# Kernel optimization log

Measured on AMD Instinct MI355X. Metric: run time of the kernel, lower is better.

Reference implementation:

```python
import jax, jax.numpy as jnp
import numpy as np

B, S, D, H = 2, 2048, 1024, 16
HD = D // H


def setup_inputs() -> dict:
    key = jax.random.key(0)
    ks = jax.random.split(key, 6)
    std = 1.0 / np.sqrt(D)
    return {
        "hidden_states": jax.random.normal(ks[0], (B, S, D), dtype=jnp.float32),
        "attention_mask": jnp.zeros((B, 1, S, S), dtype=jnp.float32),
        "Wq": jax.random.normal(ks[1], (D, D), dtype=jnp.float32) * std,
        "bq": jnp.zeros((D,), dtype=jnp.float32),
        "Wk": jax.random.normal(ks[2], (D, D), dtype=jnp.float32) * std,
        "bk": jnp.zeros((D,), dtype=jnp.float32),
        "Wv": jax.random.normal(ks[3], (D, D), dtype=jnp.float32) * std,
        "bv": jnp.zeros((D,), dtype=jnp.float32),
        "Wo": jax.random.normal(ks[4], (D, D), dtype=jnp.float32) * std,
        "bo": jnp.zeros((D,), dtype=jnp.float32),
    }


def reference(hidden_states, attention_mask, Wq, bq, Wk, bk, Wv, bv, Wo, bo):
    scale = HD ** (-0.5)
    # torch Linear: y = x @ W^T + b
    def proj(x, W, b):
        y = jnp.einsum('bsd,ed->bse', x, W) + b
        return y.reshape(B, S, H, HD).transpose(0, 2, 1, 3)  # [B,H,S,HD]
    q = proj(hidden_states, Wq, bq)
    k = proj(hidden_states, Wk, bk)
    v = proj(hidden_states, Wv, bv)
    scores = jnp.einsum('bhqd,bhkd->bhqk', q, k) * scale + attention_mask
    attn = jax.nn.softmax(scores, axis=-1)  # dropout p=0.0 -> identity
    out = jnp.einsum('bhqk,bhkd->bhqd', attn, v)
    out = out.transpose(0, 2, 1, 3).reshape(B, S, D)
    return jnp.einsum('bsd,ed->bse', out, Wo) + bo
```

## Files before the change

kernel.cpp:

```cpp
#include <hip/hip_runtime.h>
#include <hip/hip_bf16.h>
#include <stdint.h>

#define Bb 2
#define Ss 2048
#define Dd 1024
#define Hh 16
#define HD 64

typedef __attribute__((ext_vector_type(8))) __bf16 bf16x8;
typedef __attribute__((ext_vector_type(4))) __bf16 bf16x4;
typedef __attribute__((ext_vector_type(2))) __bf16 bf16x2;
typedef __attribute__((ext_vector_type(4))) float f32x4;
typedef __attribute__((ext_vector_type(16))) float f32x16;

#define LOG2E 1.44269504088896f
#define SCL2 (0.125f * LOG2E)

#define HS_N   (Bb * Ss * Dd)
#define W_N    (Dd * Dd)
#define B_N    (Dd)
#define MS_N   ((long)Bb * Ss * Ss)
#define CAN_HS 0
#define CAN_WQ (CAN_HS + HS_N)
#define CAN_BQ (CAN_WQ + W_N)
#define CAN_WK (CAN_BQ + B_N)
#define CAN_BK (CAN_WK + W_N)
#define CAN_WV (CAN_BK + B_N)
#define CAN_BV (CAN_WV + W_N)
#define CAN_WO (CAN_BV + B_N)
#define CAN_BO (CAN_WO + W_N)
#define CAN_END (CAN_BO + B_N)
#define TSZ    (Bb * Hh * Ss * HD)
#define WS_ELEMS (CAN_END + 4 * TSZ)
#define WS_NEED ((size_t)WS_ELEMS * 2)

__device__ __forceinline__ void gl_lds16(const __bf16* g, __bf16* l) {
  __builtin_amdgcn_global_load_lds(
      (const __attribute__((address_space(1))) void*)g,
      (__attribute__((address_space(3))) void*)l,
      16, 0, 0);
}

__device__ __forceinline__ void cfence() { asm volatile("" ::: "memory"); }

__global__ void canon_kernel(const float* hs, const float* Wq, const float* bq,
                             const float* Wk, const float* bk, const float* Wv,
                             const float* bv, const float* Wo, const float* bo,
                             __bf16* __restrict__ dst,
                             const float* __restrict__ Mf,
                             __bf16* __restrict__ mout) {
  const float* srcs[9] = {hs, Wq, bq, Wk, bk, Wv, bv, Wo, bo};
  const long starts[10] = {CAN_HS, CAN_WQ, CAN_BQ, CAN_WK, CAN_BK,
                           CAN_WV, CAN_BV, CAN_WO, CAN_BO, CAN_END};
  const long nA = CAN_END / 8;
  const long nTot = nA + MS_N / 8;
  for (long c = blockIdx.x * blockDim.x + threadIdx.x; c < nTot;
       c += (long)gridDim.x * blockDim.x) {
    if (c < nA) {
      const long i = c * 8;
      int seg = 0;
#pragma unroll
      for (int t = 1; t < 9; t++) seg += (i >= starts[t]) ? 1 : 0;
      const float* s = srcs[seg] + (i - starts[seg]);
      bf16x8 v;
#pragma unroll
      for (int e = 0; e < 8; e++) v[e] = (__bf16)s[e];
      *(bf16x8*)(dst + i) = v;
    } else {
      const long i = (c - nA) * 8;
      const float* s = Mf + i;
      bf16x8 v;
#pragma unroll
      for (int e = 0; e < 8; e++) v[e] = (__bf16)(s[e] * LOG2E);
      *(bf16x8*)(mout + i) = v;
    }
  }
}

template <int MODE, typename OutT>
__global__ __launch_bounds__(256, 2) void gemm_bt(
    const __bf16* __restrict__ A,
    const __bf16* __restrict__ W0, const __bf16* __restrict__ W1,
    const __bf16* __restrict__ W2,
    const __bf16* __restrict__ b0, const __bf16* __restrict__ b1,
    const __bf16* __restrict__ b2,
    OutT* __restrict__ O0, OutT* __restrict__ O1, OutT* __restrict__ O2) {
  __shared__ __align__(16) __bf16 sA[2][128 * 32];
  __shared__ __align__(16) __bf16 sB[2][128 * 32];
  const int tid = threadIdx.x;
  const int lane = tid & 63;
  const int wid = tid >> 6;
  const int quad = lane >> 4;
  const int l15 = lane & 15;
  const int mBlock = blockIdx.x * 128;

  const __bf16* W;
  const __bf16* bias;
  OutT* Out;
  int nBlock, which = 0;
  if (MODE == 0) {
    which = blockIdx.y >> 3;
    nBlock = (blockIdx.y & 7) * 128;
    W = which == 0 ? W0 : (which == 1 ? W1 : W2);
    bias = which == 0 ? b0 : (which == 1 ? b1 : b2);
    Out = which == 0 ? O0 : (which == 1 ? O1 : O2);
  } else {
    nBlock = blockIdx.y * 128;
    W = W0;
    bias = b0;
    Out = O0;
  }

  const int waveM = (wid >> 1) * 64;
  const int waveN = (wid & 1) * 64;

  f32x4 acc[4][4] = {};

  const int c1 = wid * 64 + lane;
  const int c2 = c1 + 256;
  const __bf16* Ar1 = A + (mBlock + (c1 >> 2)) * Dd + (c1 & 3) * 8;
  const __bf16* Ar2 = A + (mBlock + (c2 >> 2)) * Dd + (c2 & 3) * 8;
  const __bf16* Wr1 = W + (nBlock + (c1 >> 2)) * Dd + (c1 & 3) * 8;
  const __bf16* Wr2 = W + (nBlock + (c2 >> 2)) * Dd + (c2 & 3) * 8;
  const int d1 = (wid * 64) * 8;
  const int d2 = (wid * 64 + 256) * 8;

#define GSTAGE(BI, K0)                                                        \
  {                                                                           \
    gl_lds16(Ar1 + (K0), sA[BI] + d1);                                        \
    gl_lds16(Ar2 + (K0), sA[BI] + d2);                                        \
    gl_lds16(Wr1 + (K0), sB[BI] + d1);                                        \
    gl_lds16(Wr2 + (K0), sB[BI] + d2);                                        \
  }

  GSTAGE(0, 0);

#pragma unroll 2
  for (int kt = 0; kt < 32; ++kt) {
    const int bufc = kt & 1;
    __syncthreads();
    if (kt < 31) {
      GSTAGE(bufc ^ 1, (kt + 1) * 32);
    }

    bf16x8 aF[4], bF[4];
#pragma unroll
    for (int mi = 0; mi < 4; mi++)
      aF[mi] =
          *(const bf16x8*)(sA[bufc] + (waveM + mi * 16 + l15) * 32 + quad * 8);
#pragma unroll
    for (int ni = 0; ni < 4; ni++)
      bF[ni] =
          *(const bf16x8*)(sB[bufc] + (waveN + ni * 16 + l15) * 32 + quad * 8);
#pragma unroll
    for (int mi = 0; mi < 4; mi++)
#pragma unroll
      for (int ni = 0; ni < 4; ni++)
        acc[mi][ni] = __builtin_amdgcn_mfma_f32_16x16x32_bf16(
            aF[mi], bF[ni], acc[mi][ni], 0, 0, 0);
  }

#pragma unroll
  for (int ni = 0; ni < 4; ni++) {
    const int ng = nBlock + waveN + ni * 16 + l15;
    const float bv = (float)bias[ng];
#pragma unroll
    for (int mi = 0; mi < 4; mi++) {
      const int mg0 = mBlock + waveM + mi * 16 + quad * 4;
      if (MODE == 0 && which == 2) {
        const int b = mg0 >> 11, s0 = mg0 & 2047;
        const int h = ng >> 6, hd = ng & 63;
        bf16x4 pk;
#pragma unroll
        for (int r = 0; r < 4; r++) pk[r] = (__bf16)(acc[mi][ni][r] + bv);
        *(bf16x4*)((__bf16*)Out + (((b * Hh + h) * HD + hd) * Ss) + s0) = pk;
      } else {
#pragma unroll
        for (int r = 0; r < 4; r++) {
          float v = acc[mi][ni][r] + bv;
          const int m = mg0 + r;
          if (MODE == 0) {
            if (which == 0) v *= SCL2;
            const int b = m >> 11, s = m & 2047;
            const int h = ng >> 6, hd = ng & 63;
            Out[(((b * Hh + h) * Ss + s) * HD) + hd] = (OutT)v;
          } else {
            Out[m * Dd + ng] = (OutT)v;
          }
        }
      }
    }
  }
}

__global__ __launch_bounds__(256, 4) void attn_fused(
    const __bf16* __restrict__ Qg, const __bf16* __restrict__ Kg,
    const __bf16* __restrict__ Vt, const __bf16* __restrict__ Mbf,
    __bf16* __restrict__ Og) {
  __shared__ __align__(16) union {
    struct {
      __bf16 kv[2][8192];
      __bf16 mk[4096];
    } s;
    struct {
      float O[2][64][32];
      float L[2][32];
    } m;
  } sh;

  const int tid = threadIdx.x;
  const int lane = tid & 63;
  const int wid = tid >> 6;
  const int qg = wid & 1;
  const int kvh = wid >> 1;
  const int l31 = lane & 31;
  const int hi = lane >> 5;

  const int id = blockIdx.x;
  const int j = id >> 3;
  const int bh = (id & 7) * 4 + (j >> 5);
  const int qb0 = (j & 31) * 64;
  const int b = bh >> 4;
  const int h = bh & 15;
  const int qw = qb0 + qg * 32 + l31;

  const __bf16* Qp = Qg + (size_t)bh * Ss * HD;
  const __bf16* Kp = Kg + (size_t)bh * Ss * HD;
  const __bf16* Vp = Vt + (size_t)bh * HD * Ss;
  const __bf16* Mb = Mbf + (size_t)b * Ss * Ss;

  bf16x8 qf[4];
#pragma unroll
  for (int k = 0; k < 4; k++)
    qf[k] = *(const bf16x8*)(Qp + (size_t)qw * HD + k * 16 + hi * 8);

  const int cA = tid, cB = 256 + tid;
#define STAGE_KV(BI, KVS)                                                     \
  {                                                                           \
    const int rwA = (cA & 255) >> 2, rwB = (cB & 255) >> 2;                   \
    const int slA = (cA & 3) ^ ((rwA >> 1) & 3);                              \
    const int slB = (cB & 3) ^ ((rwB >> 1) & 3);                              \
    __bf16* kb = sh.s.kv[BI];                                                 \
    gl_lds16(Kp + ((KVS) + rwA) * HD + (cA >> 8) * 32 + slA * 8, kb + cA * 8);\
    gl_lds16(Kp + ((KVS) + rwB) * HD + (cB >> 8) * 32 + slB * 8, kb + cB * 8);\
    __bf16* vb = sh.s.kv[BI] + 4096;                                          \
    gl_lds16(Vp + (size_t)rwA * Ss + (KVS) + (cA >> 8) * 32 + slA * 8,        \
             vb + cA * 8);                                                    \
    gl_lds16(Vp + (size_t)rwB * Ss + (KVS) + (cB >> 8) * 32 + slB * 8,        \
             vb + cB * 8);                                                    \
  }

#define STAGE_M(KVS)                                                          \
  {                                                                           \
    _Pragma("unroll")                                                         \
    for (int rr = 0; rr < 2; rr++) {                                          \
      const int c = tid + rr * 256;                                           \
      const int mq = c >> 3;                                                  \
      const int l8 = (c & 7) ^ (mq & 7);                                      \
      gl_lds16(Mb + (size_t)(qb0 + mq) * Ss + (KVS) + l8 * 8,                 \
               sh.s.mk + c * 8);                                              \
    }                                                                         \
  }

  f32x16 o[2] = {};
  f32x4 lacc = {0.f, 0.f, 0.f, 0.f};

  const int rsw = (l31 >> 1) & 3;

  STAGE_KV(0, 0);
  STAGE_M(0);

  for (int it = 0; it < 32; ++it) {
    const int bufc = it & 1;
    cfence();
    asm volatile("s_waitcnt vmcnt(0)" ::: "memory");
    cfence();
    __builtin_amdgcn_s_barrier();
    cfence();
    if (it < 31) {
      STAGE_KV(bufc ^ 1, (it + 1) * 64);
      cfence();
    }

    bf16x4 mcv[4];
    const int mq = qg * 32 + l31;
#pragma unroll
    for (int g = 0; g < 4; g++) {
      const int p8 = (4 * kvh + g) ^ (l31 & 7);
      mcv[g] = *(const bf16x4*)(sh.s.mk + mq * 64 + p8 * 8 + 4 * hi);
    }
    cfence();
    asm volatile("s_waitcnt lgkmcnt(0)" ::: "memory");
    cfence();
    __builtin_amdgcn_s_barrier();
    cfence();
    if (it < 31) {
      STAGE_M((it + 1) * 64);
      cfence();
    }

    f32x16 sacc;
#pragma unroll
    for (int g = 0; g < 4; g++)
#pragma unroll
      for (int r = 0; r < 4; r++) sacc[g * 4 + r] = (float)mcv[g][r];
    __builtin_amdgcn_s_setprio(1);
#pragma unroll
    for (int k = 0; k < 4; k++) {
      const int ps = (((k & 1) << 1) | hi) ^ rsw;
      bf16x8 kf = *(const bf16x8*)(sh.s.kv[bufc] +
                                   ((k >> 1) * 64 + kvh * 32 + l31) * 32 +
                                   ps * 8);
      sacc = __builtin_amdgcn_mfma_f32_32x32x16_bf16(kf, qf[k], sacc, 0, 0, 0);
    }
    __builtin_amdgcn_s_setprio(0);

    f32x4 sv[4];
#pragma unroll
    for (int g = 0; g < 4; g++)
#pragma unroll
      for (int r = 0; r < 4; r++)
        sv[g][r] = __builtin_amdgcn_exp2f(sacc[g * 4 + r]);
    lacc += (sv[0] + sv[1]) + (sv[2] + sv[3]);

    union pu { bf16x4 v; uint32_t w[2]; };
    pu pk[4];
#pragma unroll
    for (int g = 0; g < 4; g++)
#pragma unroll
      for (int r = 0; r < 4; r++) pk[g].v[r] = (__bf16)sv[g][r];
    union PF { bf16x8 v; uint32_t u[4]; } pf[2];
#pragma unroll
    for (int ks = 0; ks < 2; ks++) {
      uint32_t a0 = pk[2 * ks].w[0], b0 = pk[2 * ks + 1].w[0];
      uint32_t a1 = pk[2 * ks].w[1], b1 = pk[2 * ks + 1].w[1];
      asm volatile("s_nop 1\n\tv_permlane32_swap_b32 %0, %1"
                   : "+v"(a0), "+v"(b0));
      asm volatile("s_nop 1\n\tv_permlane32_swap_b32 %0, %1"
                   : "+v"(a1), "+v"(b1));
      pf[ks].u[0] = a0;
      pf[ks].u[1] = a1;
      pf[ks].u[2] = b0;
      pf[ks].u[3] = b1;
    }

    __builtin_amdgcn_s_setprio(1);
#pragma unroll
    for (int k = 0; k < 2; k++)
#pragma unroll
      for (int hb = 0; hb < 2; hb++) {
        const int ps = ((k << 1) | hi) ^ rsw;
        bf16x8 vf = *(const bf16x8*)(sh.s.kv[bufc] + 4096 +
                                     (kvh * 64 + hb * 32 + l31) * 32 +
                                     ps * 8);
        o[hb] = __builtin_amdgcn_mfma_f32_32x32x16_bf16(vf, pf[k].v, o[hb],
                                                        0, 0, 0);
      }
    __builtin_amdgcn_s_setprio(0);
  }

  float l = lacc[0] + lacc[1] + lacc[2] + lacc[3];
  l += __shfl_xor(l, 32);

  __syncthreads();
  if (kvh == 1) {
#pragma unroll
    for (int hb = 0; hb < 2; hb++)
#pragma unroll
      for (int r = 0; r < 16; r++) {
        const int hd = hb * 32 + (r & 3) + 8 * (r >> 2) + 4 * hi;
        sh.m.O[qg][hd][l31] = o[hb][r];
      }
    if (hi == 0) sh.m.L[qg][l31] = l;
  }
  __syncthreads();
  if (kvh == 0) {
#pragma unroll
    for (int hb = 0; hb < 2; hb++)
#pragma unroll
      for (int r = 0; r < 16; r++) {
        const int hd = hb * 32 + (r & 3) + 8 * (r >> 2) + 4 * hi;
        o[hb][r] += sh.m.O[qg][hd][l31];
      }
    l += sh.m.L[qg][l31];
    const float inv = 1.0f / l;
    __bf16* Ow = Og + (((size_t)b * Ss + qw) * Hh + h) * HD;
#pragma unroll
    for (int hb = 0; hb < 2; hb++)
#pragma unroll
      for (int g = 0; g < 4; g++) {
        const int hd = hb * 32 + g * 8 + 4 * hi;
        bf16x2 w0, w1;
        w0[0] = (__bf16)(o[hb][g * 4 + 0] * inv);
        w0[1] = (__bf16)(o[hb][g * 4 + 1] * inv);
        w1[0] = (__bf16)(o[hb][g * 4 + 2] * inv);
        w1[1] = (__bf16)(o[hb][g * 4 + 3] * inv);
        *(bf16x2*)(Ow + hd) = w0;
        *(bf16x2*)(Ow + hd + 2) = w1;
      }
  }
}

extern "C" void kernel_launch(void* const* d_in, const int* in_sizes, int n_in,
                              void* d_out, int out_size, void* d_ws,
                              size_t ws_size, hipStream_t stream) {
  if (ws_size < WS_NEED) return;

  __bf16* ws = (__bf16*)d_ws;
  const __bf16* hsC = ws + CAN_HS;
  const __bf16* WqC = ws + CAN_WQ;
  const __bf16* bqC = ws + CAN_BQ;
  const __bf16* WkC = ws + CAN_WK;
  const __bf16* bkC = ws + CAN_BK;
  const __bf16* WvC = ws + CAN_WV;
  const __bf16* bvC = ws + CAN_BV;
  const __bf16* WoC = ws + CAN_WO;
  const __bf16* boC = ws + CAN_BO;
  __bf16* Q = ws + CAN_END;
  __bf16* K = Q + TSZ;
  __bf16* V = K + TSZ;
  __bf16* AW = V + TSZ;
  float* out = (float*)d_out;
  __bf16* Mbf = (__bf16*)d_out;

  canon_kernel<<<2048, 256, 0, stream>>>(
      (const float*)d_in[0], (const float*)d_in[2], (const float*)d_in[3],
      (const float*)d_in[4], (const float*)d_in[5], (const float*)d_in[6],
      (const float*)d_in[7], (const float*)d_in[8], (const float*)d_in[9], ws,
      (const float*)d_in[1], Mbf);
  gemm_bt<0, __bf16><<<dim3(32, 24), 256, 0, stream>>>(
      hsC, WqC, WkC, WvC, bqC, bkC, bvC, Q, K, V);
  attn_fused<<<dim3(1024), 256, 0, stream>>>(Q, K, V, Mbf, AW);
  gemm_bt<1, float><<<dim3(32, 8), 256, 0, stream>>>(
      AW, WoC, WoC, WoC, boC, boC, boC, out, out, out);
}
```

Before: 226.4 us.

## Overlap mask conversion with QKV GEMM and narrow output-GEMM tiles

The fp32-to-bf16 mask conversion moves out of the canonicalisation kernel into 256 extra blocks of the QKV projection GEMM, so it runs alongside the matmul blocks instead of serially before them. Separately, the output projection GEMM uses 128x64 tiles instead of 128x128, doubling its grid from 256 to 512 blocks to fill more compute units. The trade-off is lower per-block data reuse in the output GEMM, and mask blocks competing with GEMM blocks for bandwidth and scheduling slots.

```diff
diff --git a/kernel.cpp b/kernel.cpp
--- a/kernel.cpp
+++ b/kernel.cpp
@@ -47,34 +47,22 @@
 __global__ void canon_kernel(const float* hs, const float* Wq, const float* bq,
                              const float* Wk, const float* bk, const float* Wv,
                              const float* bv, const float* Wo, const float* bo,
-                             __bf16* __restrict__ dst,
-                             const float* __restrict__ Mf,
-                             __bf16* __restrict__ mout) {
+                             __bf16* __restrict__ dst) {
   const float* srcs[9] = {hs, Wq, bq, Wk, bk, Wv, bv, Wo, bo};
   const long starts[10] = {CAN_HS, CAN_WQ, CAN_BQ, CAN_WK, CAN_BK,
                            CAN_WV, CAN_BV, CAN_WO, CAN_BO, CAN_END};
   const long nA = CAN_END / 8;
-  const long nTot = nA + MS_N / 8;
-  for (long c = blockIdx.x * blockDim.x + threadIdx.x; c < nTot;
+  for (long c = blockIdx.x * blockDim.x + threadIdx.x; c < nA;
        c += (long)gridDim.x * blockDim.x) {
-    if (c < nA) {
-      const long i = c * 8;
-      int seg = 0;
-#pragma unroll
-      for (int t = 1; t < 9; t++) seg += (i >= starts[t]) ? 1 : 0;
-      const float* s = srcs[seg] + (i - starts[seg]);
-      bf16x8 v;
-#pragma unroll
-      for (int e = 0; e < 8; e++) v[e] = (__bf16)s[e];
-      *(bf16x8*)(dst + i) = v;
-    } else {
-      const long i = (c - nA) * 8;
-      const float* s = Mf + i;
-      bf16x8 v;
-#pragma unroll
-      for (int e = 0; e < 8; e++) v[e] = (__bf16)(s[e] * LOG2E);
-      *(bf16x8*)(mout + i) = v;
-    }
+    const long i = c * 8;
+    int seg = 0;
+#pragma unroll
+    for (int t = 1; t < 9; t++) seg += (i >= starts[t]) ? 1 : 0;
+    const float* s = srcs[seg] + (i - starts[seg]);
+    bf16x8 v;
+#pragma unroll
+    for (int e = 0; e < 8; e++) v[e] = (__bf16)s[e];
+    *(bf16x8*)(dst + i) = v;
   }
 }
 
@@ -85,10 +73,27 @@
     const __bf16* __restrict__ W2,
     const __bf16* __restrict__ b0, const __bf16* __restrict__ b1,
     const __bf16* __restrict__ b2,
-    OutT* __restrict__ O0, OutT* __restrict__ O1, OutT* __restrict__ O2) {
+    OutT* __restrict__ O0, OutT* __restrict__ O1, OutT* __restrict__ O2,
+    const float* __restrict__ Mf, __bf16* __restrict__ Mout) {
+  constexpr int TN = (MODE == 1) ? 64 : 128;
+  constexpr int NACC = TN / 32;
   __shared__ __align__(16) __bf16 sA[2][128 * 32];
-  __shared__ __align__(16) __bf16 sB[2][128 * 32];
+  __shared__ __align__(16) __bf16 sB[2][TN * 32];
   const int tid = threadIdx.x;
+
+  if (MODE == 0 && blockIdx.y >= 24) {
+    const long nC = MS_N / 8;
+    const long c0 = ((long)(blockIdx.y - 24) * 32 + blockIdx.x) * 256 + tid;
+    for (long c = c0; c < nC; c += 65536) {
+      const float* s = Mf + c * 8;
+      bf16x8 v;
+#pragma unroll
+      for (int e = 0; e < 8; e++) v[e] = (__bf16)(s[e] * LOG2E);
+      *(bf16x8*)(Mout + c * 8) = v;
+    }
+    return;
+  }
+
   const int lane = tid & 63;
   const int wid = tid >> 6;
   const int quad = lane >> 4;
@@ -106,16 +111,16 @@
     bias = which == 0 ? b0 : (which == 1 ? b1 : b2);
     Out = which == 0 ? O0 : (which == 1 ? O1 : O2);
   } else {
-    nBlock = blockIdx.y * 128;
+    nBlock = blockIdx.y * TN;
     W = W0;
     bias = b0;
     Out = O0;
   }
 
   const int waveM = (wid >> 1) * 64;
-  const int waveN = (wid & 1) * 64;
-
-  f32x4 acc[4][4] = {};
+  const int waveN = (wid & 1) * (TN / 2);
+
+  f32x4 acc[4][NACC] = {};
 
   const int c1 = wid * 64 + lane;
   const int c2 = c1 + 256;
@@ -131,7 +136,7 @@
     gl_lds16(Ar1 + (K0), sA[BI] + d1);                                        \
     gl_lds16(Ar2 + (K0), sA[BI] + d2);                                        \
     gl_lds16(Wr1 + (K0), sB[BI] + d1);                                        \
-    gl_lds16(Wr2 + (K0), sB[BI] + d2);                                        \
+    if (MODE == 0) gl_lds16(Wr2 + (K0), sB[BI] + d2);                         \
   }
 
   GSTAGE(0, 0);
@@ -144,25 +149,25 @@
       GSTAGE(bufc ^ 1, (kt + 1) * 32);
     }
 
-    bf16x8 aF[4], bF[4];
+    bf16x8 aF[4], bF[NACC];
 #pragma unroll
     for (int mi = 0; mi < 4; mi++)
       aF[mi] =
           *(const bf16x8*)(sA[bufc] + (waveM + mi * 16 + l15) * 32 + quad * 8);
 #pragma unroll
-    for (int ni = 0; ni < 4; ni++)
+    for (int ni = 0; ni < NACC; ni++)
       bF[ni] =
           *(const bf16x8*)(sB[bufc] + (waveN + ni * 16 + l15) * 32 + quad * 8);
 #pragma unroll
     for (int mi = 0; mi < 4; mi++)
 #pragma unroll
-      for (int ni = 0; ni < 4; ni++)
+      for (int ni = 0; ni < NACC; ni++)
         acc[mi][ni] = __builtin_amdgcn_mfma_f32_16x16x32_bf16(
             aF[mi], bF[ni], acc[mi][ni], 0, 0, 0);
   }
 
 #pragma unroll
-  for (int ni = 0; ni < 4; ni++) {
+  for (int ni = 0; ni < NACC; ni++) {
     const int ng = nBlock + waveN + ni * 16 + l15;
     const float bv = (float)bias[ng];
 #pragma unroll
@@ -427,11 +432,10 @@
   canon_kernel<<<2048, 256, 0, stream>>>(
       (const float*)d_in[0], (const float*)d_in[2], (const float*)d_in[3],
       (const float*)d_in[4], (const float*)d_in[5], (const float*)d_in[6],
-      (const float*)d_in[7], (const float*)d_in[8], (const float*)d_in[9], ws,
-      (const float*)d_in[1], Mbf);
-  gemm_bt<0, __bf16><<<dim3(32, 24), 256, 0, stream>>>(
-      hsC, WqC, WkC, WvC, bqC, bkC, bvC, Q, K, V);
+      (const float*)d_in[7], (const float*)d_in[8], (const float*)d_in[9], ws);
+  gemm_bt<0, __bf16><<<dim3(32, 32), 256, 0, stream>>>(
+      hsC, WqC, WkC, WvC, bqC, bkC, bvC, Q, K, V, (const float*)d_in[1], Mbf);
   attn_fused<<<dim3(1024), 256, 0, stream>>>(Q, K, V, Mbf, AW);
-  gemm_bt<1, float><<<dim3(32, 8), 256, 0, stream>>>(
-      AW, WoC, WoC, WoC, boC, boC, boC, out, out, out);
+  gemm_bt<1, float><<<dim3(32, 16), 256, 0, stream>>>(
+      AW, WoC, WoC, WoC, boC, boC, boC, out, out, out, nullptr, nullptr);
 }
```

New measurement: 222.6 us. Within noise of the previous version (-1.7%).
